# Kernel optimization log

Measured on AMD Instinct MI355X. Metric: run time of the kernel, lower is better.

Reference implementation:

```python
import jax, jax.numpy as jnp
import numpy as np

B_, L_, D_, E_, N_, DT_, K_ = 2, 1024, 1024, 2048, 16, 64, 4
EPS = 1e-5


def setup_inputs() -> dict:
    key = jax.random.key(0)
    ks = jax.random.split(key, 16)
    s = lambda *sh: 1.0 / np.sqrt(sh[-1])
    return {
        "resid": jax.random.normal(ks[0], (B_, L_, D_), jnp.float32),
        "norm_w": jnp.ones((D_,), jnp.float32),
        "skip_w": jax.random.normal(ks[1], (E_, D_), jnp.float32) * s(E_, D_),
        "in_w": jax.random.normal(ks[2], (E_, D_), jnp.float32) * s(E_, D_),
        "conv_w": jax.random.normal(ks[3], (E_, K_), jnp.float32) * s(E_, K_),
        "conv_b": jax.random.normal(ks[4], (E_,), jnp.float32) * 0.1,
        "wd1": jax.random.normal(ks[5], (DT_, E_), jnp.float32) * s(DT_, E_),
        "wd2": jax.random.normal(ks[6], (E_, DT_), jnp.float32) * s(E_, DT_),
        "wd2_b": jax.random.normal(ks[7], (E_,), jnp.float32) * 0.1,
        "wb": jax.random.normal(ks[8], (N_, E_), jnp.float32) * s(N_, E_),
        "wc": jax.random.normal(ks[9], (N_, E_), jnp.float32) * s(N_, E_),
        "A_log": jnp.log(jax.random.uniform(ks[10], (E_, N_), jnp.float32, 0.5, 4.0)),
        "W_D": jnp.ones((E_,), jnp.float32),
        "out_w": jax.random.normal(ks[11], (D_, E_), jnp.float32) * s(D_, E_),
    }


def _forward(resid, norm_w, skip_w, in_w, conv_w, conv_b, wd1, wd2, wd2_b,
             wb, wc, A_log, W_D, out_w):
    B, L, D = resid.shape
    E, N = A_log.shape
    K = conv_w.shape[-1]
    # RMSNorm
    xn = resid * jax.lax.rsqrt(jnp.mean(resid * resid, -1, keepdims=True) + EPS) * norm_w
    skip = jnp.einsum('bld,ed->ble', xn, skip_w)
    x = jnp.einsum('bld,ed->ble', xn, in_w)
    # causal depthwise conv1d (torch pads both sides by K-1, output cut to [:L])
    xp = jnp.pad(x, ((0, 0), (K - 1, 0), (0, 0)))
    conv = conv_b + sum(xp[:, k:k + L, :] * conv_w[:, k] for k in range(K))
    x = jax.nn.silu(conv)  # [B,L,E] ssm input
    # input-dependent projections
    delta = jax.nn.softplus(jnp.einsum('ble,re->blr', x, wd1) @ wd2.T + wd2_b)  # [B,L,E]
    Bt = jnp.einsum('ble,ne->bln', x, wb)  # [B,L,N]
    Ct = jnp.einsum('ble,ne->bln', x, wc)  # [B,L,N]
    A = -jnp.exp(A_log)  # [E,N]

    def step(h, inp):
        dt, b_t, c_t, x_t = inp  # [B,E],[B,N],[B,N],[B,E]
        A_bar = jnp.exp(dt[:, :, None] * A)          # [B,E,N]
        h = A_bar * h + (dt * x_t)[:, :, None] * b_t[:, None, :]
        y = jnp.einsum('ben,bn->be', h, c_t)
        return h, y

    h0 = jnp.zeros((B, E, N), x.dtype)
    xs = (delta.transpose(1, 0, 2), Bt.transpose(1, 0, 2),
          Ct.transpose(1, 0, 2), x.transpose(1, 0, 2))
    _, y = jax.lax.scan(step, h0, xs)
    y = y.transpose(1, 0, 2)  # [B,L,E]
    y = y + x * W_D
    y = y * jax.nn.silu(skip)
    y = jnp.einsum('ble,de->bld', y, out_w)
    return resid + y


def reference(resid, norm_w, skip_w, in_w, conv_w, conv_b, wd1, wd2, wd2_b,
              wb, wc, A_log, W_D, out_w):
    return _forward(resid, norm_w, skip_w, in_w, conv_w, conv_b, wd1, wd2,
                    wd2_b, wb, wc, A_log, W_D, out_w)
```

## Files before the change

kernel.cpp:

```cpp
#include <hip/hip_runtime.h>
#include <cstdint>

typedef unsigned short u16;
typedef float f32x4 __attribute__((ext_vector_type(4)));
typedef __bf16 bf16x8 __attribute__((ext_vector_type(8)));
typedef u16 u16x8 __attribute__((ext_vector_type(8)));

__device__ __forceinline__ u16 f2bf(float f) {
  uint32_t u = __float_as_uint(f);
  u += 0x7fffu + ((u >> 16) & 1u);
  return (u16)(u >> 16);
}
__device__ __forceinline__ float bf2f(u16 s) {
  return __uint_as_float(((uint32_t)s) << 16);
}

__device__ __forceinline__ void ld16(const u16* g, u16* l) {
  auto* gp = reinterpret_cast<const __attribute__((address_space(1))) u16*>(
      reinterpret_cast<uintptr_t>(g));
  auto* lp = reinterpret_cast<__attribute__((address_space(3))) u16*>(
      static_cast<uint32_t>(reinterpret_cast<uintptr_t>(l)));
  __builtin_amdgcn_global_load_lds(gp, lp, 16, 0, 0);
}

__device__ __forceinline__ f32x4 mfma16(u16x8 a, u16x8 b, f32x4 c) {
  return __builtin_amdgcn_mfma_f32_16x16x32_bf16(
      __builtin_bit_cast(bf16x8, a), __builtin_bit_cast(bf16x8, b), c, 0, 0, 0);
}

__device__ __forceinline__ float sigmoidf_(float x) { return 1.f / (1.f + __expf(-x)); }
__device__ __forceinline__ float siluf_(float x) { return x * sigmoidf_(x); }
__device__ __forceinline__ float softplusf_(float x) {
  return fmaxf(x, 0.f) + log1pf(__expf(-fabsf(x)));
}

#define PACK_TOT 6651904
__global__ __launch_bounds__(256) void pack_kernel(
    const float* __restrict__ skip_w, const float* __restrict__ in_w,
    const float* __restrict__ out_w, const float* __restrict__ wd2,
    const float* __restrict__ wd1, const float* __restrict__ wb,
    const float* __restrict__ wc, const float* __restrict__ A_log,
    u16* __restrict__ skipw_bf, u16* __restrict__ inw_bf, u16* __restrict__ outw_bf,
    u16* __restrict__ wd2_bf, u16* __restrict__ w96, float* __restrict__ Aneg) {
  int stride = gridDim.x * 256;
  for (int i = blockIdx.x * 256 + threadIdx.x; i < PACK_TOT; i += stride) {
    int j = i;
    if (j < 2097152) { skipw_bf[j] = f2bf(skip_w[j]); continue; } j -= 2097152;
    if (j < 2097152) { inw_bf[j] = f2bf(in_w[j]); continue; } j -= 2097152;
    if (j < 2097152) { outw_bf[j] = f2bf(out_w[j]); continue; } j -= 2097152;
    if (j < 131072)  { wd2_bf[j] = f2bf(wd2[j]); continue; } j -= 131072;
    if (j < 131072)  { w96[j] = f2bf(wd1[j]); continue; } j -= 131072;
    if (j < 32768)   { w96[131072 + j] = f2bf(wb[j]); continue; } j -= 32768;
    if (j < 32768)   { w96[163840 + j] = f2bf(wc[j]); continue; } j -= 32768;
    Aneg[j] = -__expf(A_log[j]);
  }
}

__global__ __launch_bounds__(256) void rmsnorm_kernel(
    const float* __restrict__ x, const float* __restrict__ w, u16* __restrict__ out) {
  int row = blockIdx.x, t = threadIdx.x;
  const float4* xr = (const float4*)(x + (size_t)row * 1024);
  float4 v = xr[t];
  float ss = v.x * v.x + v.y * v.y + v.z * v.z + v.w * v.w;
  for (int o = 32; o > 0; o >>= 1) ss += __shfl_xor(ss, o);
  __shared__ float wsum[4];
  if ((t & 63) == 0) wsum[t >> 6] = ss;
  __syncthreads();
  float tot = wsum[0] + wsum[1] + wsum[2] + wsum[3];
  float rs = rsqrtf(tot * (1.0f / 1024.0f) + 1e-5f);
  float4 wv = ((const float4*)w)[t];
  uint2 pk;
  pk.x = (uint32_t)f2bf(v.x * rs * wv.x) | ((uint32_t)f2bf(v.y * rs * wv.y) << 16);
  pk.y = (uint32_t)f2bf(v.z * rs * wv.z) | ((uint32_t)f2bf(v.w * rs * wv.w) << 16);
  ((uint2*)out)[row * 256 + t] = pk;
}

template <int BM, int BN, int BK, int EPI>
__global__ __launch_bounds__(256) void gemm_bt(
    const u16* __restrict__ A, const u16* __restrict__ B0, const u16* __restrict__ B1,
    int M, int N, int K, int Nsplit,
    void* __restrict__ C0, void* __restrict__ C1,
    const float* __restrict__ bias, const float* __restrict__ addsrc) {
  constexpr int TM = BM / 32, TN = BN / 32;
  constexpr int KC = BK / 8;
  __shared__ __align__(16) u16 sA[BM * BK];
  __shared__ __align__(16) u16 sB[BN * BK];
  const int t = threadIdx.x;
  const int lane = t & 63, wid = t >> 6;
  const int wm = wid >> 1, wn = wid & 1;
  const int mBase = blockIdx.y * BM;
  const int nBase = blockIdx.x * BN;
  const bool hi = (nBase >= Nsplit);
  const u16* Bp = hi ? B1 : B0;
  const int nB0 = nBase - (hi ? Nsplit : 0);
  const int col = lane & 15, quad = lane >> 4;

  f32x4 acc[TM][TN];
#pragma unroll
  for (int i = 0; i < TM; ++i)
#pragma unroll
    for (int j = 0; j < TN; ++j) acc[i][j] = f32x4{0.f, 0.f, 0.f, 0.f};

  for (int k0 = 0; k0 < K; k0 += BK) {
#pragma unroll
    for (int c = t; c < BM * KC; c += 256) {
      int row = c / KC, k8 = (c % KC) * 8;
      ld16(A + (size_t)(mBase + row) * K + k0 + k8, &sA[c * 8]);
    }
#pragma unroll
    for (int c = t; c < BN * KC; c += 256) {
      int row = c / KC, k8 = (c % KC) * 8;
      ld16(Bp + (size_t)(nB0 + row) * K + k0 + k8, &sB[c * 8]);
    }
    __syncthreads();
#pragma unroll
    for (int kk = 0; kk < BK / 32; ++kk) {
      u16x8 af[TM], bfv[TN];
#pragma unroll
      for (int i = 0; i < TM; ++i)
        af[i] = *(const u16x8*)&sA[(wm * (BM / 2) + i * 16 + col) * BK + kk * 32 + quad * 8];
#pragma unroll
      for (int j = 0; j < TN; ++j)
        bfv[j] = *(const u16x8*)&sB[(wn * (BN / 2) + j * 16 + col) * BK + kk * 32 + quad * 8];
#pragma unroll
      for (int i = 0; i < TM; ++i)
#pragma unroll
        for (int j = 0; j < TN; ++j) acc[i][j] = mfma16(af[i], bfv[j], acc[i][j]);
    }
    __syncthreads();
  }

#pragma unroll
  for (int i = 0; i < TM; ++i) {
#pragma unroll
    for (int j = 0; j < TN; ++j) {
#pragma unroll
      for (int r = 0; r < 4; ++r) {
        int gm = mBase + wm * (BM / 2) + i * 16 + quad * 4 + r;
        int gn = nBase + wn * (BN / 2) + j * 16 + col;
        float v = acc[i][j][r];
        if (EPI == 0) {
          if (gn < Nsplit)
            ((u16*)C0)[(size_t)gm * Nsplit + gn] = f2bf(v);
          else
            ((u16*)C1)[(size_t)gm * (N - Nsplit) + (gn - Nsplit)] = f2bf(v);
        } else if (EPI == 1) {
          ((u16*)C0)[(size_t)gm * N + gn] = f2bf(softplusf_(v + bias[gn]));
        } else {
          ((float*)C0)[(size_t)gm * N + gn] = addsrc[(size_t)gm * N + gn] + v;
        }
      }
    }
  }
}

__global__ __launch_bounds__(256) void gemm_skinny_splitk(
    const u16* __restrict__ A, const u16* __restrict__ B,
    float* __restrict__ part) {
  __shared__ __align__(16) u16 sA[64 * 32];
  __shared__ __align__(16) u16 sB[96 * 32];
  const int t = threadIdx.x, lane = t & 63, w = t >> 6;
  const int mBase = blockIdx.x * 64;
  const int kBase = blockIdx.y * 256;
  const int col = lane & 15, quad = lane >> 4;
  const int K = 2048;
  f32x4 acc[6];
#pragma unroll
  for (int j = 0; j < 6; ++j) acc[j] = f32x4{0.f, 0.f, 0.f, 0.f};

  for (int k0 = kBase; k0 < kBase + 256; k0 += 32) {
    for (int c = t; c < 640; c += 256) {
      if (c < 256) {
        int row = c >> 2, k8 = (c & 3) * 8;
        ld16(A + (size_t)(mBase + row) * K + k0 + k8, &sA[c * 8]);
      } else {
        int cb = c - 256;
        int row = cb >> 2, k8 = (cb & 3) * 8;
        ld16(B + (size_t)row * K + k0 + k8, &sB[cb * 8]);
      }
    }
    __syncthreads();
    u16x8 af = *(const u16x8*)&sA[(w * 16 + col) * 32 + quad * 8];
#pragma unroll
    for (int j = 0; j < 6; ++j) {
      u16x8 bfv = *(const u16x8*)&sB[(j * 16 + col) * 32 + quad * 8];
      acc[j] = mfma16(af, bfv, acc[j]);
    }
    __syncthreads();
  }
  float* pp = part + (size_t)blockIdx.y * (2048 * 96);
#pragma unroll
  for (int j = 0; j < 6; ++j)
#pragma unroll
    for (int r = 0; r < 4; ++r) {
      int gm = mBase + w * 16 + quad * 4 + r;
      int gn = j * 16 + col;
      pp[gm * 96 + gn] = acc[j][r];
    }
}

__global__ __launch_bounds__(256) void skinny_reduce(
    const float* __restrict__ part, u16* __restrict__ d1_bf,
    float* __restrict__ bc) {
  int i = blockIdx.x * 256 + threadIdx.x;
  float s = 0.f;
#pragma unroll
  for (int kc = 0; kc < 8; ++kc) s += part[kc * 196608 + i];
  int m = i / 96, n = i - m * 96;
  if (n < 64) d1_bf[m * 64 + n] = f2bf(s);
  else bc[m * 32 + n - 64] = s;
}

__global__ __launch_bounds__(256) void conv_silu_kernel(
    const u16* __restrict__ xin_bf, const float* __restrict__ conv_w,
    const float* __restrict__ conv_b, u16* __restrict__ xconv_bf) {
  int i = blockIdx.x * 256 + threadIdx.x;
  int e = i & 2047;
  int l = (i >> 11) & 1023;
  float4 wv = ((const float4*)conv_w)[e];
  float acc = conv_b[e] + bf2f(xin_bf[i]) * wv.w;
  if (l >= 1) acc += bf2f(xin_bf[i - 2048]) * wv.z;
  if (l >= 2) acc += bf2f(xin_bf[i - 4096]) * wv.y;
  if (l >= 3) acc += bf2f(xin_bf[i - 6144]) * wv.x;
  xconv_bf[i] = f2bf(siluf_(acc));
}

__global__ __launch_bounds__(256) void scan1_kernel(
    const u16* __restrict__ delta_bf, const u16* __restrict__ xconv_bf,
    const float* __restrict__ bc, const float* __restrict__ Aneg,
    float* __restrict__ hloc, float* __restrict__ Ssum) {
  int t = threadIdx.x;
  int e = blockIdx.x * 256 + t;
  int c = blockIdx.y, b = blockIdx.z;
  int m0 = b * 1024 + c * 32;
  __shared__ float sBC[1024];
  for (int j = t; j < 1024; j += 256) sBC[j] = bc[m0 * 32 + j];
  float Ar[16], h[16];
#pragma unroll
  for (int n = 0; n < 16; ++n) { Ar[n] = Aneg[e * 16 + n]; h[n] = 0.f; }
  float S = 0.f;
  __syncthreads();
  for (int l = 0; l < 32; ++l) {
    size_t m = (size_t)(m0 + l) * 2048 + e;
    float dt = bf2f(delta_bf[m]), xv = bf2f(xconv_bf[m]);
    S += dt;
    float dx = dt * xv;
    const float* bl = &sBC[l * 32];
#pragma unroll
    for (int n = 0; n < 16; ++n) h[n] = __expf(dt * Ar[n]) * h[n] + dx * bl[n];
  }
  size_t base = ((size_t)(b * 32 + c) * 2048 + e) * 16;
#pragma unroll
  for (int n = 0; n < 16; ++n) hloc[base + n] = h[n];
  Ssum[(b * 32 + c) * 2048 + e] = S;
}

__global__ __launch_bounds__(256) void combine_kernel(
    const float* __restrict__ Aneg, const float* __restrict__ Ssum,
    float* __restrict__ hloc) {
  int tid = blockIdx.x * 256 + threadIdx.x;
  int b = tid >> 15, r = tid & 32767;
  int e = r >> 4;
  float a = Aneg[r];
  float h = 0.f;
  for (int c = 0; c < 32; ++c) {
    size_t base = (size_t)(b * 32 + c) * 32768 + r;
    float hl = hloc[base];
    float S = Ssum[(b * 32 + c) * 2048 + e];
    hloc[base] = h;
    h = __expf(a * S) * h + hl;
  }
}

__global__ __launch_bounds__(256) void scan2_kernel(
    const u16* __restrict__ delta_bf, const u16* __restrict__ xconv_bf,
    const float* __restrict__ bc, const float* __restrict__ Aneg,
    const float* __restrict__ hloc, const u16* __restrict__ skip_bf,
    const float* __restrict__ W_D, u16* __restrict__ yfin_bf) {
  int t = threadIdx.x;
  int e = blockIdx.x * 256 + t;
  int c = blockIdx.y, b = blockIdx.z;
  int m0 = b * 1024 + c * 32;
  __shared__ float sBC[1024];
  for (int j = t; j < 1024; j += 256) sBC[j] = bc[m0 * 32 + j];
  float Ar[16], h[16];
  size_t hbase = ((size_t)(b * 32 + c) * 2048 + e) * 16;
#pragma unroll
  for (int n = 0; n < 16; ++n) { Ar[n] = Aneg[e * 16 + n]; h[n] = hloc[hbase + n]; }
  float wd = W_D[e];
  __syncthreads();
  for (int l = 0; l < 32; ++l) {
    size_t m = (size_t)(m0 + l) * 2048 + e;
    float dt = bf2f(delta_bf[m]), xv = bf2f(xconv_bf[m]);
    float dx = dt * xv;
    const float* bl = &sBC[l * 32];
    float y = 0.f;
#pragma unroll
    for (int n = 0; n < 16; ++n) {
      h[n] = __expf(dt * Ar[n]) * h[n] + dx * bl[n];
      y += h[n] * bl[16 + n];
    }
    float yv = y + xv * wd;
    float sk = bf2f(skip_bf[m]);
    yv *= sk * sigmoidf_(sk);
    yfin_bf[m] = f2bf(yv);
  }
}

extern "C" void kernel_launch(void* const* d_in, const int* in_sizes, int n_in,
                              void* d_out, int out_size, void* d_ws, size_t ws_size,
                              hipStream_t stream) {
  (void)in_sizes; (void)n_in; (void)out_size; (void)ws_size;
  const float* resid  = (const float*)d_in[0];
  const float* norm_w = (const float*)d_in[1];
  const float* skip_w = (const float*)d_in[2];
  const float* in_w   = (const float*)d_in[3];
  const float* conv_w = (const float*)d_in[4];
  const float* conv_b = (const float*)d_in[5];
  const float* wd1    = (const float*)d_in[6];
  const float* wd2    = (const float*)d_in[7];
  const float* wd2_b  = (const float*)d_in[8];
  const float* wb     = (const float*)d_in[9];
  const float* wc     = (const float*)d_in[10];
  const float* A_log  = (const float*)d_in[11];
  const float* W_D    = (const float*)d_in[12];
  const float* out_w  = (const float*)d_in[13];

  char* p = (char*)d_ws;
  u16*   skipw_bf = (u16*)(p + 0);
  u16*   inw_bf   = (u16*)(p + 4194304);
  u16*   outw_bf  = (u16*)(p + 8388608);
  u16*   wd2_bf   = (u16*)(p + 12582912);
  u16*   w96      = (u16*)(p + 12845056);
  float* Aneg     = (float*)(p + 13238272);
  u16*   xn_bf    = (u16*)(p + 13369344);
  u16*   skip_bf  = (u16*)(p + 17563648);
  u16*   xin_bf   = (u16*)(p + 25952256);
  u16*   xconv_bf = (u16*)(p + 34340864);
  u16*   delta_bf = (u16*)(p + 42729472);
  u16*   d1_bf    = (u16*)(p + 51118080);
  float* bc       = (float*)(p + 51380224);
  u16*   yfin_bf  = (u16*)(p + 51642368);
  float* part     = (float*)(p + 60030976);
  float* hloc     = (float*)(p + 66322432);
  float* Ssum     = (float*)(p + 74711040);

  pack_kernel<<<8192, 256, 0, stream>>>(skip_w, in_w, out_w, wd2, wd1, wb, wc, A_log,
                                        skipw_bf, inw_bf, outw_bf, wd2_bf, w96, Aneg);
  rmsnorm_kernel<<<2048, 256, 0, stream>>>(resid, norm_w, xn_bf);
  gemm_bt<128, 128, 32, 0><<<dim3(32, 16), 256, 0, stream>>>(
      xn_bf, skipw_bf, inw_bf, 2048, 4096, 1024, 2048,
      (void*)skip_bf, (void*)xin_bf, nullptr, nullptr);
  conv_silu_kernel<<<16384, 256, 0, stream>>>(xin_bf, conv_w, conv_b, xconv_bf);
  gemm_skinny_splitk<<<dim3(32, 8), 256, 0, stream>>>(xconv_bf, w96, part);
  skinny_reduce<<<768, 256, 0, stream>>>(part, d1_bf, bc);
  gemm_bt<128, 128, 64, 1><<<dim3(16, 16), 256, 0, stream>>>(
      d1_bf, wd2_bf, wd2_bf, 2048, 2048, 64, 2048,
      (void*)delta_bf, nullptr, wd2_b, nullptr);
  scan1_kernel<<<dim3(8, 32, 2), 256, 0, stream>>>(delta_bf, xconv_bf, bc, Aneg,
                                                   hloc, Ssum);
  combine_kernel<<<256, 256, 0, stream>>>(Aneg, Ssum, hloc);
  scan2_kernel<<<dim3(8, 32, 2), 256, 0, stream>>>(delta_bf, xconv_bf, bc, Aneg, hloc,
                                                   skip_bf, W_D, yfin_bf);
  gemm_bt<64, 64, 64, 2><<<dim3(16, 32), 256, 0, stream>>>(
      yfin_bf, outw_bf, outw_bf, 2048, 1024, 2048, 1024,
      (void*)d_out, nullptr, nullptr, resid);
}
```

Baseline: 262.0 us.

## Fuse pack with rmsnorm, fuse conv into skinny GEMM, swizzle LDS, retune BK

Merges the weight-packing and RMSNorm kernels into one launch, and fuses the causal depthwise conv plus SiLU into the skinny split-K GEMM so the conv output is written to LDS and consumed directly. Adds a rotation swizzle on the LDS k-chunk layout in the generic GEMM to cut bank conflicts. Raises BK for the input-projection and output GEMMs. This removes launches and a global round trip of the conv output, at the cost of more LDS use and fewer blocks doing the conv work.

After: 232.5 us. 11.3% less time.

```diff
diff --git a/kernel.cpp b/kernel.cpp
--- a/kernel.cpp
+++ b/kernel.cpp
@@ -35,15 +35,36 @@
 }
 
 #define PACK_TOT 6651904
-__global__ __launch_bounds__(256) void pack_kernel(
+__global__ __launch_bounds__(256) void pack_rms_kernel(
     const float* __restrict__ skip_w, const float* __restrict__ in_w,
     const float* __restrict__ out_w, const float* __restrict__ wd2,
     const float* __restrict__ wd1, const float* __restrict__ wb,
     const float* __restrict__ wc, const float* __restrict__ A_log,
     u16* __restrict__ skipw_bf, u16* __restrict__ inw_bf, u16* __restrict__ outw_bf,
-    u16* __restrict__ wd2_bf, u16* __restrict__ w96, float* __restrict__ Aneg) {
-  int stride = gridDim.x * 256;
-  for (int i = blockIdx.x * 256 + threadIdx.x; i < PACK_TOT; i += stride) {
+    u16* __restrict__ wd2_bf, u16* __restrict__ w96, float* __restrict__ Aneg,
+    const float* __restrict__ resid, const float* __restrict__ norm_w,
+    u16* __restrict__ xn_bf) {
+  int t = threadIdx.x;
+  if (blockIdx.x >= 1024) {
+    int row = blockIdx.x - 1024;
+    const float4* xr = (const float4*)(resid + (size_t)row * 1024);
+    float4 v = xr[t];
+    float ss = v.x * v.x + v.y * v.y + v.z * v.z + v.w * v.w;
+    for (int o = 32; o > 0; o >>= 1) ss += __shfl_xor(ss, o);
+    __shared__ float wsum[4];
+    if ((t & 63) == 0) wsum[t >> 6] = ss;
+    __syncthreads();
+    float tot = wsum[0] + wsum[1] + wsum[2] + wsum[3];
+    float rs = rsqrtf(tot * (1.0f / 1024.0f) + 1e-5f);
+    float4 wv = ((const float4*)norm_w)[t];
+    uint2 pk;
+    pk.x = (uint32_t)f2bf(v.x * rs * wv.x) | ((uint32_t)f2bf(v.y * rs * wv.y) << 16);
+    pk.y = (uint32_t)f2bf(v.z * rs * wv.z) | ((uint32_t)f2bf(v.w * rs * wv.w) << 16);
+    ((uint2*)xn_bf)[row * 256 + t] = pk;
+    return;
+  }
+  const int stride = 1024 * 256;
+  for (int i = blockIdx.x * 256 + t; i < PACK_TOT; i += stride) {
     int j = i;
     if (j < 2097152) { skipw_bf[j] = f2bf(skip_w[j]); continue; } j -= 2097152;
     if (j < 2097152) { inw_bf[j] = f2bf(in_w[j]); continue; } j -= 2097152;
@@ -54,25 +75,6 @@
     if (j < 32768)   { w96[163840 + j] = f2bf(wc[j]); continue; } j -= 32768;
     Aneg[j] = -__expf(A_log[j]);
   }
-}
-
-__global__ __launch_bounds__(256) void rmsnorm_kernel(
-    const float* __restrict__ x, const float* __restrict__ w, u16* __restrict__ out) {
-  int row = blockIdx.x, t = threadIdx.x;
-  const float4* xr = (const float4*)(x + (size_t)row * 1024);
-  float4 v = xr[t];
-  float ss = v.x * v.x + v.y * v.y + v.z * v.z + v.w * v.w;
-  for (int o = 32; o > 0; o >>= 1) ss += __shfl_xor(ss, o);
-  __shared__ float wsum[4];
-  if ((t & 63) == 0) wsum[t >> 6] = ss;
-  __syncthreads();
-  float tot = wsum[0] + wsum[1] + wsum[2] + wsum[3];
-  float rs = rsqrtf(tot * (1.0f / 1024.0f) + 1e-5f);
-  float4 wv = ((const float4*)w)[t];
-  uint2 pk;
-  pk.x = (uint32_t)f2bf(v.x * rs * wv.x) | ((uint32_t)f2bf(v.y * rs * wv.y) << 16);
-  pk.y = (uint32_t)f2bf(v.z * rs * wv.z) | ((uint32_t)f2bf(v.w * rs * wv.w) << 16);
-  ((uint2*)out)[row * 256 + t] = pk;
 }
 
 template <int BM, int BN, int BK, int EPI>
@@ -104,12 +106,14 @@
   for (int k0 = 0; k0 < K; k0 += BK) {
 #pragma unroll
     for (int c = t; c < BM * KC; c += 256) {
-      int row = c / KC, k8 = (c % KC) * 8;
+      int row = c / KC, j = c % KC;
+      int k8 = ((j + row) & (KC - 1)) * 8;
       ld16(A + (size_t)(mBase + row) * K + k0 + k8, &sA[c * 8]);
     }
 #pragma unroll
     for (int c = t; c < BN * KC; c += 256) {
-      int row = c / KC, k8 = (c % KC) * 8;
+      int row = c / KC, j = c % KC;
+      int k8 = ((j + row) & (KC - 1)) * 8;
       ld16(Bp + (size_t)(nB0 + row) * K + k0 + k8, &sB[c * 8]);
     }
     __syncthreads();
@@ -117,11 +121,15 @@
     for (int kk = 0; kk < BK / 32; ++kk) {
       u16x8 af[TM], bfv[TN];
 #pragma unroll
-      for (int i = 0; i < TM; ++i)
-        af[i] = *(const u16x8*)&sA[(wm * (BM / 2) + i * 16 + col) * BK + kk * 32 + quad * 8];
-#pragma unroll
-      for (int j = 0; j < TN; ++j)
-        bfv[j] = *(const u16x8*)&sB[(wn * (BN / 2) + j * 16 + col) * BK + kk * 32 + quad * 8];
+      for (int i = 0; i < TM; ++i) {
+        int rowA = wm * (BM / 2) + i * 16 + col;
+        af[i] = *(const u16x8*)&sA[rowA * BK + (((kk * 4 + quad) - rowA) & (KC - 1)) * 8];
+      }
+#pragma unroll
+      for (int j = 0; j < TN; ++j) {
+        int rowB = wn * (BN / 2) + j * 16 + col;
+        bfv[j] = *(const u16x8*)&sB[rowB * BK + (((kk * 4 + quad) - rowB) & (KC - 1)) * 8];
+      }
 #pragma unroll
       for (int i = 0; i < TM; ++i)
 #pragma unroll
@@ -154,39 +162,85 @@
   }
 }
 
-__global__ __launch_bounds__(256) void gemm_skinny_splitk(
-    const u16* __restrict__ A, const u16* __restrict__ B,
-    float* __restrict__ part) {
-  __shared__ __align__(16) u16 sA[64 * 32];
-  __shared__ __align__(16) u16 sB[96 * 32];
+__global__ __launch_bounds__(256) void conv_skinny_kernel(
+    const u16* __restrict__ xin_bf, const float* __restrict__ conv_w,
+    const float* __restrict__ conv_b, u16* __restrict__ xconv_bf,
+    const u16* __restrict__ w96, float* __restrict__ part) {
+  constexpr int PAD = 264;
+  __shared__ __align__(16) u16 sA[64 * PAD];
+  __shared__ __align__(16) u16 sB[96 * 128];
   const int t = threadIdx.x, lane = t & 63, w = t >> 6;
   const int mBase = blockIdx.x * 64;
-  const int kBase = blockIdx.y * 256;
+  const int e0 = blockIdx.y * 256;
+
+  {
+    const int ep = (t & 127) * 2;
+    const int strip = t >> 7;
+    const int ms = mBase + strip * 32;
+    const int l0 = ms & 1023;
+    const uint32_t* xr = (const uint32_t*)xin_bf;
+    size_t base = ((size_t)ms * 2048 + e0 + ep) >> 1;
+    int eg = e0 + ep;
+    float4 w0 = ((const float4*)conv_w)[eg];
+    float4 w1 = ((const float4*)conv_w)[eg + 1];
+    float b0 = conv_b[eg], b1 = conv_b[eg + 1];
+    uint32_t u;
+    u = (l0 >= 1) ? xr[base - 1024] : 0u;
+    float h10 = bf2f((u16)u), h11 = bf2f((u16)(u >> 16));
+    u = (l0 >= 2) ? xr[base - 2048] : 0u;
+    float h20 = bf2f((u16)u), h21 = bf2f((u16)(u >> 16));
+    u = (l0 >= 3) ? xr[base - 3072] : 0u;
+    float h30 = bf2f((u16)u), h31 = bf2f((u16)(u >> 16));
+#pragma unroll 4
+    for (int r = 0; r < 32; ++r) {
+      uint32_t ux = xr[base + (size_t)r * 1024];
+      float x0 = bf2f((u16)ux), x1 = bf2f((u16)(ux >> 16));
+      float a0 = b0 + w0.w * x0 + w0.z * h10 + w0.y * h20 + w0.x * h30;
+      float a1 = b1 + w1.w * x1 + w1.z * h11 + w1.y * h21 + w1.x * h31;
+      a0 = siluf_(a0); a1 = siluf_(a1);
+      uint32_t pk = (uint32_t)f2bf(a0) | ((uint32_t)f2bf(a1) << 16);
+      ((uint32_t*)xconv_bf)[base + (size_t)r * 1024] = pk;
+      *(uint32_t*)&sA[(strip * 32 + r) * PAD + ep] = pk;
+      h30 = h20; h31 = h21; h20 = h10; h21 = h11; h10 = x0; h11 = x1;
+    }
+  }
+  for (int c = t; c < 96 * 16; c += 256) {
+    int row = c >> 4, j = c & 15;
+    int k8 = ((j + row) & 15) * 8;
+    ld16(w96 + (size_t)row * 2048 + e0 + k8, &sB[c * 8]);
+  }
+  __syncthreads();
   const int col = lane & 15, quad = lane >> 4;
-  const int K = 2048;
+  const int rowA = w * 16 + col;
   f32x4 acc[6];
 #pragma unroll
   for (int j = 0; j < 6; ++j) acc[j] = f32x4{0.f, 0.f, 0.f, 0.f};
-
-  for (int k0 = kBase; k0 < kBase + 256; k0 += 32) {
-    for (int c = t; c < 640; c += 256) {
-      if (c < 256) {
-        int row = c >> 2, k8 = (c & 3) * 8;
-        ld16(A + (size_t)(mBase + row) * K + k0 + k8, &sA[c * 8]);
-      } else {
-        int cb = c - 256;
-        int row = cb >> 2, k8 = (cb & 3) * 8;
-        ld16(B + (size_t)row * K + k0 + k8, &sB[cb * 8]);
-      }
-    }
-    __syncthreads();
-    u16x8 af = *(const u16x8*)&sA[(w * 16 + col) * 32 + quad * 8];
+#pragma unroll
+  for (int kk = 0; kk < 4; ++kk) {
+    u16x8 af = *(const u16x8*)&sA[rowA * PAD + kk * 32 + quad * 8];
 #pragma unroll
     for (int j = 0; j < 6; ++j) {
-      u16x8 bfv = *(const u16x8*)&sB[(j * 16 + col) * 32 + quad * 8];
+      int rowB = j * 16 + col;
+      u16x8 bfv = *(const u16x8*)&sB[rowB * 128 + (((kk * 4 + quad) - rowB) & 15) * 8];
       acc[j] = mfma16(af, bfv, acc[j]);
     }
-    __syncthreads();
+  }
+  __syncthreads();
+  for (int c = t; c < 96 * 16; c += 256) {
+    int row = c >> 4, j = c & 15;
+    int k8 = ((j + row) & 15) * 8;
+    ld16(w96 + (size_t)row * 2048 + e0 + 128 + k8, &sB[c * 8]);
+  }
+  __syncthreads();
+#pragma unroll
+  for (int kk = 4; kk < 8; ++kk) {
+    u16x8 af = *(const u16x8*)&sA[rowA * PAD + kk * 32 + quad * 8];
+#pragma unroll
+    for (int j = 0; j < 6; ++j) {
+      int rowB = j * 16 + col;
+      u16x8 bfv = *(const u16x8*)&sB[rowB * 128 + ((((kk - 4) * 4 + quad) - rowB) & 15) * 8];
+      acc[j] = mfma16(af, bfv, acc[j]);
+    }
   }
   float* pp = part + (size_t)blockIdx.y * (2048 * 96);
 #pragma unroll
@@ -209,20 +263,6 @@
   int m = i / 96, n = i - m * 96;
   if (n < 64) d1_bf[m * 64 + n] = f2bf(s);
   else bc[m * 32 + n - 64] = s;
-}
-
-__global__ __launch_bounds__(256) void conv_silu_kernel(
-    const u16* __restrict__ xin_bf, const float* __restrict__ conv_w,
-    const float* __restrict__ conv_b, u16* __restrict__ xconv_bf) {
-  int i = blockIdx.x * 256 + threadIdx.x;
-  int e = i & 2047;
-  int l = (i >> 11) & 1023;
-  float4 wv = ((const float4*)conv_w)[e];
-  float acc = conv_b[e] + bf2f(xin_bf[i]) * wv.w;
-  if (l >= 1) acc += bf2f(xin_bf[i - 2048]) * wv.z;
-  if (l >= 2) acc += bf2f(xin_bf[i - 4096]) * wv.y;
-  if (l >= 3) acc += bf2f(xin_bf[i - 6144]) * wv.x;
-  xconv_bf[i] = f2bf(siluf_(acc));
 }
 
 __global__ __launch_bounds__(256) void scan1_kernel(
@@ -345,14 +385,15 @@
   float* hloc     = (float*)(p + 66322432);
   float* Ssum     = (float*)(p + 74711040);
 
-  pack_kernel<<<8192, 256, 0, stream>>>(skip_w, in_w, out_w, wd2, wd1, wb, wc, A_log,
-                                        skipw_bf, inw_bf, outw_bf, wd2_bf, w96, Aneg);
-  rmsnorm_kernel<<<2048, 256, 0, stream>>>(resid, norm_w, xn_bf);
-  gemm_bt<128, 128, 32, 0><<<dim3(32, 16), 256, 0, stream>>>(
+  pack_rms_kernel<<<3072, 256, 0, stream>>>(
+      skip_w, in_w, out_w, wd2, wd1, wb, wc, A_log,
+      skipw_bf, inw_bf, outw_bf, wd2_bf, w96, Aneg,
+      resid, norm_w, xn_bf);
+  gemm_bt<128, 128, 64, 0><<<dim3(32, 16), 256, 0, stream>>>(
       xn_bf, skipw_bf, inw_bf, 2048, 4096, 1024, 2048,
       (void*)skip_bf, (void*)xin_bf, nullptr, nullptr);
-  conv_silu_kernel<<<16384, 256, 0, stream>>>(xin_bf, conv_w, conv_b, xconv_bf);
-  gemm_skinny_splitk<<<dim3(32, 8), 256, 0, stream>>>(xconv_bf, w96, part);
+  conv_skinny_kernel<<<dim3(32, 8), 256, 0, stream>>>(
+      xin_bf, conv_w, conv_b, xconv_bf, w96, part);
   skinny_reduce<<<768, 256, 0, stream>>>(part, d1_bf, bc);
   gemm_bt<128, 128, 64, 1><<<dim3(16, 16), 256, 0, stream>>>(
       d1_bf, wd2_bf, wd2_bf, 2048, 2048, 64, 2048,
@@ -362,7 +403,7 @@
   combine_kernel<<<256, 256, 0, stream>>>(Aneg, Ssum, hloc);
   scan2_kernel<<<dim3(8, 32, 2), 256, 0, stream>>>(delta_bf, xconv_bf, bc, Aneg, hloc,
                                                    skip_bf, W_D, yfin_bf);
-  gemm_bt<64, 64, 64, 2><<<dim3(16, 32), 256, 0, stream>>>(
+  gemm_bt<64, 64, 128, 2><<<dim3(16, 32), 256, 0, stream>>>(
       yfin_bf, outw_bf, outw_bf, 2048, 1024, 2048, 1024,
       (void*)d_out, nullptr, nullptr, resid);
 }
```
